# Optimization experiments

Measured on AMD Instinct MI355X. Metric: run time of the kernel, lower is better.

## Reference

```python
import jax, jax.numpy as jnp
import numpy as np

F_IN, F_OUT, N_HEADS = 64, 256, 4
HEAD_DIM = F_OUT // N_HEADS


def setup_inputs() -> dict:
    key = jax.random.key(0)
    ks = jax.random.split(key, 9)
    s_in = 1.0 / np.sqrt(F_IN)
    s_out = 1.0 / np.sqrt(F_OUT)
    return {
        "x": jax.random.normal(ks[0], (4, 32, F_IN, 512), dtype=jnp.float32),
        "Wq": jax.random.normal(ks[1], (F_IN, F_OUT), dtype=jnp.float32) * s_in,
        "bq": jax.random.normal(ks[2], (F_OUT,), dtype=jnp.float32) * 0.01,
        "Wk": jax.random.normal(ks[3], (F_IN, F_OUT), dtype=jnp.float32) * s_in,
        "bk": jax.random.normal(ks[4], (F_OUT,), dtype=jnp.float32) * 0.01,
        "Wv": jax.random.normal(ks[5], (F_IN, F_OUT), dtype=jnp.float32) * s_in,
        "bv": jax.random.normal(ks[6], (F_OUT,), dtype=jnp.float32) * 0.01,
        "Wo": jax.random.normal(ks[7], (F_OUT, F_OUT), dtype=jnp.float32) * s_out,
        "bo": jax.random.normal(ks[8], (F_OUT,), dtype=jnp.float32) * 0.01,
    }


def reference(x, Wq, bq, Wk, bk, Wv, bv, Wo, bo):
    B, N, Fdim, T = x.shape
    xp = jnp.transpose(x, (0, 1, 3, 2))  # [B, N, T, F]
    q = xp @ Wq + bq  # [B, N, T, f_out]
    k = xp @ Wk + bk
    v = xp @ Wv + bv
    # split f_out into heads: [B, N, T, H, hd]
    q = q.reshape(B, N, T, N_HEADS, HEAD_DIM)
    k = k.reshape(B, N, T, N_HEADS, HEAD_DIM)
    v = v.reshape(B, N, T, N_HEADS, HEAD_DIM)
    scale = 1.0 / np.sqrt(HEAD_DIM)
    # full TxT score matrix per (batch, node, head), as in the original
    scores = jnp.einsum("bnqhd,bnkhd->bnhqk", q, k) * scale
    attn = jax.nn.softmax(scores, axis=-1)
    out = jnp.einsum("bnhqk,bnkhd->bnqhd", attn, v)  # [B, N, T, H, hd]
    out = out.reshape(B, N, T, F_OUT)  # head-concat along feature dim
    out = out @ Wo + bo  # fc_out; dropout is identity at inference
    return jnp.transpose(out, (0, 1, 3, 2))  # [B, N, f_out, T]
```

## Files before the change

kernel.cpp:

```cpp
#include <hip/hip_runtime.h>

constexpr int kT = 512;
constexpr int kF = 64;
constexpr int kC = 256;
constexpr int kH = 4;
constexpr int kHD = 64;
constexpr int kBN = 128;

typedef __attribute__((ext_vector_type(4))) float f32x4;
typedef __attribute__((ext_vector_type(8))) short s16x8;
typedef __attribute__((ext_vector_type(4))) unsigned int u32x4;

__device__ inline unsigned short f2bf(float f) {
  unsigned int u = __float_as_uint(f);
  u += 0x7fff + ((u >> 16) & 1);
  return (unsigned short)(u >> 16);
}

__device__ inline unsigned int cvt_pk(float a, float b) {
  unsigned int w;
  asm("v_cvt_pk_bf16_f32 %0, %1, %2" : "=v"(w) : "v"(a), "v"(b));
  return w;
}

__device__ inline float max3f(float a, float b, float c) {
  return fmaxf(fmaxf(a, b), c);
}

__device__ inline float exp2_hw(float x) {
  float r;
  asm("v_exp_f32 %0, %1" : "=v"(r) : "v"(x));
  return r;
}

__global__ __launch_bounds__(256) void k_prep(
    const float* __restrict__ Wq, const float* __restrict__ Wk,
    const float* __restrict__ Wv, const float* __restrict__ Wo,
    unsigned short* __restrict__ WB, unsigned short* __restrict__ WoT) {
  int i = blockIdx.x * 256 + threadIdx.x;
  const int total = 768 * 64 + 256 * 256;
  for (; i < total; i += gridDim.x * 256) {
    if (i < 768 * 64) {
      int c = i >> 6, f = i & 63;
      int arr = c >> 8, cc = c & 255;
      const float* W = (arr == 0) ? Wq : (arr == 1) ? Wk : Wv;
      WB[i] = f2bf(W[f * 256 + cc]);
    } else {
      int j = i - 768 * 64;
      int co = j >> 8, c = j & 255;
      WoT[j] = f2bf(Wo[c * 256 + co]);
    }
  }
}

__global__ __launch_bounds__(1024, 4) void k_fattn(
    const float* __restrict__ x, const unsigned short* __restrict__ WB,
    const float* __restrict__ bq, const float* __restrict__ bk,
    const float* __restrict__ bv, unsigned short* __restrict__ Aw) {
  __shared__ __align__(16) unsigned char smem[149504];
  unsigned char* Kl = smem;
  unsigned char* VtB = smem + 65536;
  unsigned char* xCb = smem + 131072;

  const int tid = threadIdx.x;
  const int bid = blockIdx.x;
  const int orig = (bid & 7) * 64 + (bid >> 3);
  const int lbn = orig >> 2;
  const int h = orig & 3;
  const int lane = tid & 63, wid = tid >> 6;
  const int lr = lane & 15, lg = lane >> 4;
  const int swz = (lr & 7) << 4;

  const float kQscale = 0.180336880111120426f;
  const unsigned short* WBq = WB + (size_t)(h * 64) * 64;
  const unsigned short* WBk = WB + (size_t)(256 + h * 64) * 64;
  const unsigned short* WBv = WB + (size_t)(512 + h * 64) * 64;

#define XFRAG(r, c) (const s16x8*)(xCb + (r) * 144 + \
    (((c) * 2) ^ ((((r) >> 2) & 7) << 4)))

  s16x8 qf[2][2];

  for (int tch = 0; tch < 4; ++tch) {
    __syncthreads();
    const float* xb = x + (size_t)lbn * kF * kT + tch * 128;
#pragma unroll
    for (int it = 0; it < 2; ++it) {
      int idx = tid + it * 1024;
      int f = idx >> 5, t4 = idx & 31;
      float4 v = *(const float4*)(xb + f * kT + t4 * 4);
      unsigned int wlo = cvt_pk(v.x, v.y);
      unsigned int whi = cvt_pk(v.z, v.w);
      const int fb = f * 2;
      const int colb = (fb & 15) | ((((fb >> 4) ^ (t4 & 7))) << 4);
      unsigned char* rp = xCb + (t4 * 4) * 144 + colb;
      *(unsigned short*)(rp + 0 * 144) = (unsigned short)wlo;
      *(unsigned short*)(rp + 1 * 144) = (unsigned short)(wlo >> 16);
      *(unsigned short*)(rp + 2 * 144) = (unsigned short)whi;
      *(unsigned short*)(rp + 3 * 144) = (unsigned short)(whi >> 16);
    }
    __syncthreads();

#pragma unroll
    for (int j = 0; j < 4; ++j) {
      const int tau = wid * 4 + j;
      const int isV = tau >> 5;
      const int tl = tau & 31;
      const int ct = tl >> 3, tt = tl & 7;
      const unsigned short* Wsrc = isV ? WBv : WBk;
      s16x8 af0 = *(const s16x8*)(Wsrc + (ct * 16 + lr) * 64 + lg * 8);
      s16x8 af1 = *(const s16x8*)(Wsrc + (ct * 16 + lr) * 64 + 32 + lg * 8);
      s16x8 bf0 = *XFRAG(tt * 16 + lr, lg * 8);
      s16x8 bf1 = *XFRAG(tt * 16 + lr, 32 + lg * 8);
      if (!isV) {
        f32x4 a = {0.f, 0.f, 0.f, 0.f};
        a = __builtin_amdgcn_mfma_f32_16x16x32_bf16(af0, bf0, a, 0, 0, 0);
        a = __builtin_amdgcn_mfma_f32_16x16x32_bf16(af1, bf1, a, 0, 0, 0);
        const int dbase = ct * 16 + lg * 4;
        const int t = tch * 128 + tt * 16 + lr;
        uint2 pk;
        pk.x = cvt_pk(a[0] + bk[h * 64 + dbase + 0],
                      a[1] + bk[h * 64 + dbase + 1]);
        pk.y = cvt_pk(a[2] + bk[h * 64 + dbase + 2],
                      a[3] + bk[h * 64 + dbase + 3]);
        *(uint2*)(Kl + ((t * 128 + dbase * 2) ^ ((t & 7) << 4))) = pk;
      } else {
        f32x4 a = {0.f, 0.f, 0.f, 0.f};
        a = __builtin_amdgcn_mfma_f32_16x16x32_bf16(bf0, af0, a, 0, 0, 0);
        a = __builtin_amdgcn_mfma_f32_16x16x32_bf16(bf1, af1, a, 0, 0, 0);
        const int d = ct * 16 + lr;
        const float bias = bv[h * 64 + d];
        const int t0 = tch * 128 + tt * 16 + lg * 4;
        const int pos0 = ((t0 >> 5) << 5) | (((t0 >> 2) & 3) << 3) |
                         (((t0 >> 4) & 1) << 2);
        uint2 pk;
        pk.x = cvt_pk(a[0] + bias, a[1] + bias);
        pk.y = cvt_pk(a[2] + bias, a[3] + bias);
        *(uint2*)(VtB + ((d * 1024 + pos0 * 2) ^ ((d & 7) << 4))) = pk;
      }
    }

    if ((wid >> 2) == tch) {
      f32x4 qa[2][4];
#pragma unroll
      for (int qt = 0; qt < 2; ++qt) {
        const int ttq = (wid & 3) * 2 + qt;
#pragma unroll
        for (int ct = 0; ct < 4; ++ct) {
          s16x8 af0 = *(const s16x8*)(WBq + (ct * 16 + lr) * 64 + lg * 8);
          s16x8 af1 = *(const s16x8*)(WBq + (ct * 16 + lr) * 64 + 32 + lg * 8);
          s16x8 bf0 = *XFRAG(ttq * 16 + lr, lg * 8);
          s16x8 bf1 = *XFRAG(ttq * 16 + lr, 32 + lg * 8);
          f32x4 a = {0.f, 0.f, 0.f, 0.f};
          a = __builtin_amdgcn_mfma_f32_16x16x32_bf16(af0, bf0, a, 0, 0, 0);
          a = __builtin_amdgcn_mfma_f32_16x16x32_bf16(af1, bf1, a, 0, 0, 0);
          const int dbase = ct * 16 + lg * 4;
#pragma unroll
          for (int r = 0; r < 4; ++r)
            a[r] = (a[r] + bq[h * 64 + dbase + r]) * kQscale;
          qa[qt][ct] = a;
        }
      }
      const int sel = lg >> 1;
#pragma unroll
      for (int qt = 0; qt < 2; ++qt)
#pragma unroll
        for (int half = 0; half < 2; ++half) {
          unsigned int w[4];
#pragma unroll
          for (int i2 = 0; i2 < 4; ++i2) {
            const int r0 = (i2 & 1) * 2;
            const int lgp = (lg & 1) * 2 + (i2 >> 1);
            const int src = lgp * 16 + lr;
            float loA = __shfl(qa[qt][half * 2 + 0][r0], src);
            float hiA = __shfl(qa[qt][half * 2 + 1][r0], src);
            float loB = __shfl(qa[qt][half * 2 + 0][r0 + 1], src);
            float hiB = __shfl(qa[qt][half * 2 + 1][r0 + 1], src);
            w[i2] = cvt_pk(sel ? hiA : loA, sel ? hiB : loB);
          }
          qf[qt][half] =
              __builtin_bit_cast(s16x8, (u32x4){w[0], w[1], w[2], w[3]});
        }
    }
  }
  __syncthreads();
#undef XFRAG

  unsigned short* Ab = Aw + (size_t)lbn * kT * kC + h * kHD;
  const int qbase = wid * 32;

  f32x4 o0[4] = {{0,0,0,0},{0,0,0,0},{0,0,0,0},{0,0,0,0}};
  f32x4 o1[4] = {{0,0,0,0},{0,0,0,0},{0,0,0,0},{0,0,0,0}};
  float m0 = -3e38f, m1 = -3e38f, l0 = 0.f, l1 = 0.f;

  const int koff = (lg * 16) ^ swz;
  const unsigned char* kp0 = Kl + lr * 128 + koff;
  const unsigned char* kp1 = Kl + lr * 128 + (koff ^ 64);
  const unsigned char* vp0 = VtB + lr * 1024 + ((lg * 16) ^ swz);
  const unsigned char* vp1 = VtB + lr * 1024 + (((lg * 16) ^ 64) ^ swz);

  unsigned int w0[8], w1[8];

#define SOFTMAX_QT(sa, m, l, o, w)                                            \
  {                                                                           \
    float g0 = max3f(sa[0][0], sa[0][1], sa[0][2]);                           \
    float g1 = max3f(sa[0][3], sa[1][0], sa[1][1]);                           \
    float g2 = max3f(sa[1][2], sa[1][3], sa[2][0]);                           \
    float g3 = max3f(sa[2][1], sa[2][2], sa[2][3]);                           \
    float g4 = max3f(sa[3][0], sa[3][1], sa[3][2]);                           \
    float tm = fmaxf(max3f(g0, g1, g2), max3f(g3, g4, sa[3][3]));             \
    if (__any(tm > m + 8.0f)) {                                               \
      tm = fmaxf(tm, __shfl_xor(tm, 16));                                     \
      tm = fmaxf(tm, __shfl_xor(tm, 32));                                     \
      float mn = fmaxf(m, tm);                                                \
      float al = exp2_hw(m - mn);                                             \
      m = mn;                                                                 \
      l *= al;                                                                \
      float aq0 = __shfl(al, (lane & 48) | (lg * 4 + 0));                     \
      float aq1 = __shfl(al, (lane & 48) | (lg * 4 + 1));                     \
      float aq2 = __shfl(al, (lane & 48) | (lg * 4 + 2));                     \
      float aq3 = __shfl(al, (lane & 48) | (lg * 4 + 3));                     \
      _Pragma("unroll")                                                       \
      for (int dt = 0; dt < 4; ++dt) {                                        \
        o[dt][0] *= aq0; o[dt][1] *= aq1;                                     \
        o[dt][2] *= aq2; o[dt][3] *= aq3;                                     \
      }                                                                       \
    }                                                                         \
    _Pragma("unroll")                                                         \
    for (int s = 0; s < 4; ++s) {                                             \
      float e0 = exp2_hw(sa[s][0] - m);                                       \
      float e1 = exp2_hw(sa[s][1] - m);                                       \
      float e2 = exp2_hw(sa[s][2] - m);                                       \
      float e3 = exp2_hw(sa[s][3] - m);                                       \
      l += (e0 + e1) + (e2 + e3);                                             \
      w[2*s]   = cvt_pk(e0, e1);                                              \
      w[2*s+1] = cvt_pk(e2, e3);                                              \
    }                                                                         \
  }

  for (int kc = 0; kc < 8; ++kc) {
    f32x4 sa0[4], sa1[4];
#pragma unroll
    for (int s = 0; s < 4; ++s) {
      s16x8 kf0 = *(const s16x8*)(kp0 + s * 2048);
      s16x8 kf1 = *(const s16x8*)(kp1 + s * 2048);
      f32x4 z0 = {0.f, 0.f, 0.f, 0.f};
      z0 = __builtin_amdgcn_mfma_f32_16x16x32_bf16(kf0, qf[0][0], z0, 0, 0, 0);
      z0 = __builtin_amdgcn_mfma_f32_16x16x32_bf16(kf1, qf[0][1], z0, 0, 0, 0);
      sa0[s] = z0;
      f32x4 z1 = {0.f, 0.f, 0.f, 0.f};
      z1 = __builtin_amdgcn_mfma_f32_16x16x32_bf16(kf0, qf[1][0], z1, 0, 0, 0);
      z1 = __builtin_amdgcn_mfma_f32_16x16x32_bf16(kf1, qf[1][1], z1, 0, 0, 0);
      sa1[s] = z1;
    }
    kp0 += 8192;
    kp1 += 8192;

    s16x8 vb0[4], vb1[4];
#pragma unroll
    for (int dt = 0; dt < 4; ++dt) {
      vb0[dt] = *(const s16x8*)(vp0 + dt * 16384);
      vb1[dt] = *(const s16x8*)(vp1 + dt * 16384);
    }
    vp0 += 128;
    vp1 += 128;

    SOFTMAX_QT(sa0, m0, l0, o0, w0)
    SOFTMAX_QT(sa1, m1, l1, o1, w1)

    s16x8 pa00 = __builtin_bit_cast(s16x8, (u32x4){w0[0], w0[1], w0[2], w0[3]});
    s16x8 pa01 = __builtin_bit_cast(s16x8, (u32x4){w0[4], w0[5], w0[6], w0[7]});
    s16x8 pa10 = __builtin_bit_cast(s16x8, (u32x4){w1[0], w1[1], w1[2], w1[3]});
    s16x8 pa11 = __builtin_bit_cast(s16x8, (u32x4){w1[4], w1[5], w1[6], w1[7]});

#pragma unroll
    for (int dt = 0; dt < 4; ++dt) {
      o0[dt] = __builtin_amdgcn_mfma_f32_16x16x32_bf16(pa00, vb0[dt], o0[dt], 0, 0, 0);
      o1[dt] = __builtin_amdgcn_mfma_f32_16x16x32_bf16(pa10, vb0[dt], o1[dt], 0, 0, 0);
    }
#pragma unroll
    for (int dt = 0; dt < 4; ++dt) {
      o0[dt] = __builtin_amdgcn_mfma_f32_16x16x32_bf16(pa01, vb1[dt], o0[dt], 0, 0, 0);
      o1[dt] = __builtin_amdgcn_mfma_f32_16x16x32_bf16(pa11, vb1[dt], o1[dt], 0, 0, 0);
    }
  }
#undef SOFTMAX_QT

#pragma unroll
  for (int qt = 0; qt < 2; ++qt) {
    float l = (qt == 0) ? l0 : l1;
    f32x4* o = (qt == 0) ? o0 : o1;
    float l2 = l + __shfl_xor(l, 16);
    float lr4 = l2 + __shfl_xor(l2, 32);
    float li0 = 1.0f / __shfl(lr4, (lane & 48) | (lg * 4 + 0));
    float li1 = 1.0f / __shfl(lr4, (lane & 48) | (lg * 4 + 1));
    float li2 = 1.0f / __shfl(lr4, (lane & 48) | (lg * 4 + 2));
    float li3 = 1.0f / __shfl(lr4, (lane & 48) | (lg * 4 + 3));
    const int qb = qbase + qt * 16;
#pragma unroll
    for (int r = 0; r < 4; ++r) {
      float li = (r == 0) ? li0 : (r == 1) ? li1 : (r == 2) ? li2 : li3;
      unsigned short* orow = Ab + (size_t)(qb + lg * 4 + r) * kC;
      unsigned int wa = cvt_pk(o[0][r] * li, o[1][r] * li);
      unsigned int wb = cvt_pk(o[2][r] * li, o[3][r] * li);
      orow[0 * 16 + lr] = (unsigned short)wa;
      orow[1 * 16 + lr] = (unsigned short)(wa >> 16);
      orow[2 * 16 + lr] = (unsigned short)wb;
      orow[3 * 16 + lr] = (unsigned short)(wb >> 16);
    }
  }
}

__global__ __launch_bounds__(512) void k_proj(
    const unsigned short* __restrict__ Aw, const unsigned short* __restrict__ WoT,
    const float* __restrict__ bo, float* __restrict__ out) {
  __shared__ __align__(16) unsigned char Al[128 * 512];

  const int tid = threadIdx.x;
  const int lbn = blockIdx.x >> 2;
  const int tch = blockIdx.x & 3;
  const int t0 = tch * 128;

  const uint4* Asrc = (const uint4*)(Aw + ((size_t)lbn * kT + t0) * kC);
#pragma unroll
  for (int i = 0; i < 8; ++i) {
    int idx = tid + i * 512;
    int trow = idx >> 5, cc = idx & 31;
    *(uint4*)(Al + ((trow * 512 + cc * 16) ^ ((trow & 7) << 4))) = Asrc[idx];
  }
  __syncthreads();

  const int lane = tid & 63, wid = tid >> 6;
  const int lr = lane & 15, lg = lane >> 4;
  const int swz = (lr & 7) << 4;
  const int tb = (wid >> 2) * 64;
  const int cob = (wid & 3) * 64;

  float* ob = out + (size_t)lbn * kC * kT;

  for (int ci = 0; ci < 4; ++ci) {
    const int co0 = cob + ci * 16;
    s16x8 af[8];
#pragma unroll
    for (int kc = 0; kc < 8; ++kc)
      af[kc] = *(const s16x8*)(WoT + (size_t)(co0 + lr) * 256 + kc * 32 + lg * 8);
    float b4[4];
#pragma unroll
    for (int r = 0; r < 4; ++r) b4[r] = bo[co0 + lg * 4 + r];

#pragma unroll
    for (int tj = 0; tj < 4; ++tj) {
      const unsigned char* ap = Al + (tb + tj * 16 + lr) * 512;
      f32x4 acc = {0.f, 0.f, 0.f, 0.f};
#pragma unroll
      for (int kc = 0; kc < 8; ++kc) {
        s16x8 bfr = *(const s16x8*)(ap + ((kc * 64 + lg * 16) ^ swz));
        acc = __builtin_amdgcn_mfma_f32_16x16x32_bf16(af[kc], bfr, acc, 0, 0, 0);
      }
      int t = t0 + tb + tj * 16 + lr;
#pragma unroll
      for (int r = 0; r < 4; ++r)
        ob[(size_t)(co0 + lg * 4 + r) * kT + t] = acc[r] + b4[r];
    }
  }
}

extern "C" void kernel_launch(void* const* d_in, const int* in_sizes, int n_in,
                              void* d_out, int out_size, void* d_ws, size_t ws_size,
                              hipStream_t stream) {
  const float* x  = (const float*)d_in[0];
  const float* Wq = (const float*)d_in[1];
  const float* bq = (const float*)d_in[2];
  const float* Wk = (const float*)d_in[3];
  const float* bk = (const float*)d_in[4];
  const float* Wv = (const float*)d_in[5];
  const float* bv = (const float*)d_in[6];
  const float* Wo = (const float*)d_in[7];
  const float* bo = (const float*)d_in[8];
  float* out = (float*)d_out;

  const size_t wElems = 768 * 64 + 256 * 256;
  const size_t aBytes = (size_t)kBN * kT * kC * 2;
  if (ws_size < wElems * 2 + aBytes) return;

  unsigned short* WB  = (unsigned short*)d_ws;
  unsigned short* WoT = WB + 768 * 64;
  unsigned short* A   = WB + wElems;

  k_prep<<<dim3(448), dim3(256), 0, stream>>>(Wq, Wk, Wv, Wo, WB, WoT);
  k_fattn<<<dim3(kBN * kH), dim3(1024), 0, stream>>>(x, WB, bq, bk, bv, A);
  k_proj<<<dim3(kBN * 4), dim3(512), 0, stream>>>(A, WoT, bo, out);
}
```

Measured before the change: 120.7 us.

## Load x fragments directly from global, drop LDS staging and block swizzle

Removes the shared-memory staging of x (and the two barriers per chunk). Each wave now gathers its bf16 MFMA B-fragments straight from global memory using strided scalar loads. Q projection is hoisted to the start so every wave computes its own Q, and the XCD-aware block index remap is dropped. s_setprio is also raised around the MFMA sections. The strided uncoalesced global loads and redundant reads of x through cache may cost more than the LDS path saved, while reduced LDS use may raise occupancy.

```diff
diff --git a/kernel.cpp b/kernel.cpp
--- a/kernel.cpp
+++ b/kernel.cpp
@@ -31,6 +31,18 @@
   float r;
   asm("v_exp_f32 %0, %1" : "=v"(r) : "v"(x));
   return r;
+}
+
+__device__ inline s16x8 xgfrag(const float* __restrict__ xb0, int trow,
+                               int fbase) {
+  unsigned int wv[4];
+#pragma unroll
+  for (int jp = 0; jp < 4; ++jp) {
+    float fa = xb0[(size_t)(fbase + 2 * jp) * kT + trow];
+    float fb = xb0[(size_t)(fbase + 2 * jp + 1) * kT + trow];
+    wv[jp] = cvt_pk(fa, fb);
+  }
+  return __builtin_bit_cast(s16x8, (u32x4){wv[0], wv[1], wv[2], wv[3]});
 }
 
 __global__ __launch_bounds__(256) void k_prep(
@@ -57,16 +69,13 @@
     const float* __restrict__ x, const unsigned short* __restrict__ WB,
     const float* __restrict__ bq, const float* __restrict__ bk,
     const float* __restrict__ bv, unsigned short* __restrict__ Aw) {
-  __shared__ __align__(16) unsigned char smem[149504];
+  __shared__ __align__(16) unsigned char smem[131072];
   unsigned char* Kl = smem;
   unsigned char* VtB = smem + 65536;
-  unsigned char* xCb = smem + 131072;
 
   const int tid = threadIdx.x;
-  const int bid = blockIdx.x;
-  const int orig = (bid & 7) * 64 + (bid >> 3);
-  const int lbn = orig >> 2;
-  const int h = orig & 3;
+  const int lbn = blockIdx.x >> 2;
+  const int h = blockIdx.x & 3;
   const int lane = tid & 63, wid = tid >> 6;
   const int lr = lane & 15, lg = lane >> 4;
   const int swz = (lr & 7) << 4;
@@ -75,32 +84,55 @@
   const unsigned short* WBq = WB + (size_t)(h * 64) * 64;
   const unsigned short* WBk = WB + (size_t)(256 + h * 64) * 64;
   const unsigned short* WBv = WB + (size_t)(512 + h * 64) * 64;
-
-#define XFRAG(r, c) (const s16x8*)(xCb + (r) * 144 + \
-    (((c) * 2) ^ ((((r) >> 2) & 7) << 4)))
+  const float* xb0 = x + (size_t)lbn * kF * kT;
+
+  const int qbase = wid * 32;
 
   s16x8 qf[2][2];
+  {
+    f32x4 qa[2][4];
+#pragma unroll
+    for (int qt = 0; qt < 2; ++qt) {
+      const int tq = qbase + qt * 16 + lr;
+      s16x8 bfr0 = xgfrag(xb0, tq, lg * 8);
+      s16x8 bfr1 = xgfrag(xb0, tq, 32 + lg * 8);
+#pragma unroll
+      for (int ct = 0; ct < 4; ++ct) {
+        s16x8 af0 = *(const s16x8*)(WBq + (ct * 16 + lr) * 64 + lg * 8);
+        s16x8 af1 = *(const s16x8*)(WBq + (ct * 16 + lr) * 64 + 32 + lg * 8);
+        f32x4 a = {0.f, 0.f, 0.f, 0.f};
+        a = __builtin_amdgcn_mfma_f32_16x16x32_bf16(af0, bfr0, a, 0, 0, 0);
+        a = __builtin_amdgcn_mfma_f32_16x16x32_bf16(af1, bfr1, a, 0, 0, 0);
+        const int dbase = ct * 16 + lg * 4;
+#pragma unroll
+        for (int r = 0; r < 4; ++r)
+          a[r] = (a[r] + bq[h * 64 + dbase + r]) * kQscale;
+        qa[qt][ct] = a;
+      }
+    }
+    const int sel = lg >> 1;
+#pragma unroll
+    for (int qt = 0; qt < 2; ++qt)
+#pragma unroll
+      for (int half = 0; half < 2; ++half) {
+        unsigned int w[4];
+#pragma unroll
+        for (int i2 = 0; i2 < 4; ++i2) {
+          const int r0 = (i2 & 1) * 2;
+          const int lgp = (lg & 1) * 2 + (i2 >> 1);
+          const int src = lgp * 16 + lr;
+          float loA = __shfl(qa[qt][half * 2 + 0][r0], src);
+          float hiA = __shfl(qa[qt][half * 2 + 1][r0], src);
+          float loB = __shfl(qa[qt][half * 2 + 0][r0 + 1], src);
+          float hiB = __shfl(qa[qt][half * 2 + 1][r0 + 1], src);
+          w[i2] = cvt_pk(sel ? hiA : loA, sel ? hiB : loB);
+        }
+        qf[qt][half] =
+            __builtin_bit_cast(s16x8, (u32x4){w[0], w[1], w[2], w[3]});
+      }
+  }
 
   for (int tch = 0; tch < 4; ++tch) {
-    __syncthreads();
-    const float* xb = x + (size_t)lbn * kF * kT + tch * 128;
-#pragma unroll
-    for (int it = 0; it < 2; ++it) {
-      int idx = tid + it * 1024;
-      int f = idx >> 5, t4 = idx & 31;
-      float4 v = *(const float4*)(xb + f * kT + t4 * 4);
-      unsigned int wlo = cvt_pk(v.x, v.y);
-      unsigned int whi = cvt_pk(v.z, v.w);
-      const int fb = f * 2;
-      const int colb = (fb & 15) | ((((fb >> 4) ^ (t4 & 7))) << 4);
-      unsigned char* rp = xCb + (t4 * 4) * 144 + colb;
-      *(unsigned short*)(rp + 0 * 144) = (unsigned short)wlo;
-      *(unsigned short*)(rp + 1 * 144) = (unsigned short)(wlo >> 16);
-      *(unsigned short*)(rp + 2 * 144) = (unsigned short)whi;
-      *(unsigned short*)(rp + 3 * 144) = (unsigned short)(whi >> 16);
-    }
-    __syncthreads();
-
 #pragma unroll
     for (int j = 0; j < 4; ++j) {
       const int tau = wid * 4 + j;
@@ -110,14 +142,15 @@
       const unsigned short* Wsrc = isV ? WBv : WBk;
       s16x8 af0 = *(const s16x8*)(Wsrc + (ct * 16 + lr) * 64 + lg * 8);
       s16x8 af1 = *(const s16x8*)(Wsrc + (ct * 16 + lr) * 64 + 32 + lg * 8);
-      s16x8 bf0 = *XFRAG(tt * 16 + lr, lg * 8);
-      s16x8 bf1 = *XFRAG(tt * 16 + lr, 32 + lg * 8);
+      const int trow = tch * 128 + tt * 16 + lr;
+      s16x8 bf0 = xgfrag(xb0, trow, lg * 8);
+      s16x8 bf1 = xgfrag(xb0, trow, 32 + lg * 8);
       if (!isV) {
         f32x4 a = {0.f, 0.f, 0.f, 0.f};
         a = __builtin_amdgcn_mfma_f32_16x16x32_bf16(af0, bf0, a, 0, 0, 0);
         a = __builtin_amdgcn_mfma_f32_16x16x32_bf16(af1, bf1, a, 0, 0, 0);
         const int dbase = ct * 16 + lg * 4;
-        const int t = tch * 128 + tt * 16 + lr;
+        const int t = trow;
         uint2 pk;
         pk.x = cvt_pk(a[0] + bk[h * 64 + dbase + 0],
                       a[1] + bk[h * 64 + dbase + 1]);
@@ -139,55 +172,10 @@
         *(uint2*)(VtB + ((d * 1024 + pos0 * 2) ^ ((d & 7) << 4))) = pk;
       }
     }
-
-    if ((wid >> 2) == tch) {
-      f32x4 qa[2][4];
-#pragma unroll
-      for (int qt = 0; qt < 2; ++qt) {
-        const int ttq = (wid & 3) * 2 + qt;
-#pragma unroll
-        for (int ct = 0; ct < 4; ++ct) {
-          s16x8 af0 = *(const s16x8*)(WBq + (ct * 16 + lr) * 64 + lg * 8);
-          s16x8 af1 = *(const s16x8*)(WBq + (ct * 16 + lr) * 64 + 32 + lg * 8);
-          s16x8 bf0 = *XFRAG(ttq * 16 + lr, lg * 8);
-          s16x8 bf1 = *XFRAG(ttq * 16 + lr, 32 + lg * 8);
-          f32x4 a = {0.f, 0.f, 0.f, 0.f};
-          a = __builtin_amdgcn_mfma_f32_16x16x32_bf16(af0, bf0, a, 0, 0, 0);
-          a = __builtin_amdgcn_mfma_f32_16x16x32_bf16(af1, bf1, a, 0, 0, 0);
-          const int dbase = ct * 16 + lg * 4;
-#pragma unroll
-          for (int r = 0; r < 4; ++r)
-            a[r] = (a[r] + bq[h * 64 + dbase + r]) * kQscale;
-          qa[qt][ct] = a;
-        }
-      }
-      const int sel = lg >> 1;
-#pragma unroll
-      for (int qt = 0; qt < 2; ++qt)
-#pragma unroll
-        for (int half = 0; half < 2; ++half) {
-          unsigned int w[4];
-#pragma unroll
-          for (int i2 = 0; i2 < 4; ++i2) {
-            const int r0 = (i2 & 1) * 2;
-            const int lgp = (lg & 1) * 2 + (i2 >> 1);
-            const int src = lgp * 16 + lr;
-            float loA = __shfl(qa[qt][half * 2 + 0][r0], src);
-            float hiA = __shfl(qa[qt][half * 2 + 1][r0], src);
-            float loB = __shfl(qa[qt][half * 2 + 0][r0 + 1], src);
-            float hiB = __shfl(qa[qt][half * 2 + 1][r0 + 1], src);
-            w[i2] = cvt_pk(sel ? hiA : loA, sel ? hiB : loB);
-          }
-          qf[qt][half] =
-              __builtin_bit_cast(s16x8, (u32x4){w[0], w[1], w[2], w[3]});
-        }
-    }
   }
   __syncthreads();
-#undef XFRAG
 
   unsigned short* Ab = Aw + (size_t)lbn * kT * kC + h * kHD;
-  const int qbase = wid * 32;
 
   f32x4 o0[4] = {{0,0,0,0},{0,0,0,0},{0,0,0,0},{0,0,0,0}};
   f32x4 o1[4] = {{0,0,0,0},{0,0,0,0},{0,0,0,0},{0,0,0,0}};
@@ -240,6 +228,7 @@
 
   for (int kc = 0; kc < 8; ++kc) {
     f32x4 sa0[4], sa1[4];
+    __builtin_amdgcn_s_setprio(1);
 #pragma unroll
     for (int s = 0; s < 4; ++s) {
       s16x8 kf0 = *(const s16x8*)(kp0 + s * 2048);
@@ -253,6 +242,7 @@
       z1 = __builtin_amdgcn_mfma_f32_16x16x32_bf16(kf1, qf[1][1], z1, 0, 0, 0);
       sa1[s] = z1;
     }
+    __builtin_amdgcn_s_setprio(0);
     kp0 += 8192;
     kp1 += 8192;
 
@@ -273,6 +263,7 @@
     s16x8 pa10 = __builtin_bit_cast(s16x8, (u32x4){w1[0], w1[1], w1[2], w1[3]});
     s16x8 pa11 = __builtin_bit_cast(s16x8, (u32x4){w1[4], w1[5], w1[6], w1[7]});
 
+    __builtin_amdgcn_s_setprio(1);
 #pragma unroll
     for (int dt = 0; dt < 4; ++dt) {
       o0[dt] = __builtin_amdgcn_mfma_f32_16x16x32_bf16(pa00, vb0[dt], o0[dt], 0, 0, 0);
@@ -283,6 +274,7 @@
       o0[dt] = __builtin_amdgcn_mfma_f32_16x16x32_bf16(pa01, vb1[dt], o0[dt], 0, 0, 0);
       o1[dt] = __builtin_amdgcn_mfma_f32_16x16x32_bf16(pa11, vb1[dt], o1[dt], 0, 0, 0);
     }
+    __builtin_amdgcn_s_setprio(0);
   }
 #undef SOFTMAX_QT
 
```

Result: slower. 123.2 us (+2.1%).
